# Kernel optimization log

Measured on AMD Instinct MI355X. Metric: run time of the kernel, lower is better.

Reference implementation:

```python
import jax, jax.numpy as jnp
import numpy as np

D = 512
H = 8
DK = D // H
EPS = 1e-5

def _layer_norm(x, w, b):
    mu = jnp.mean(x, axis=-1, keepdims=True)
    var = jnp.mean(jnp.square(x - mu), axis=-1, keepdims=True)
    return (x - mu) * jax.lax.rsqrt(var + EPS) * w + b

def setup_inputs() -> dict:
    key = jax.random.key(0)
    ks = jax.random.split(key, 16)
    B, S = 4, 2048
    s = 1.0 / np.sqrt(D)
    inp = {
        'q': jax.random.normal(ks[0], (B, S, D), jnp.float32),
        'k': jax.random.normal(ks[1], (B, S, D), jnp.float32),
        'v': jax.random.normal(ks[2], (B, S, D), jnp.float32),
        'mask': jnp.ones((S, S), jnp.int32),
        'pos_k': jax.random.normal(ks[3], (S, S), jnp.float32),
        'ln_w': jnp.ones((D,), jnp.float32),
        'ln_b': jnp.zeros((D,), jnp.float32),
        'Wq': jax.random.uniform(ks[4], (D, D), jnp.float32, -s, s),
        'bq': jax.random.uniform(ks[5], (D,), jnp.float32, -s, s),
        'Wk': jax.random.uniform(ks[6], (D, D), jnp.float32, -s, s),
        'bk': jax.random.uniform(ks[7], (D,), jnp.float32, -s, s),
        'Wv': jax.random.uniform(ks[8], (D, D), jnp.float32, -s, s),
        'bv': jax.random.uniform(ks[9], (D,), jnp.float32, -s, s),
        'Wo': jax.random.uniform(ks[10], (D, D), jnp.float32, -s, s),
        'bo': jax.random.uniform(ks[11], (D,), jnp.float32, -s, s),
    }
    return inp

def reference(q, k, v, mask, pos_k, ln_w, ln_b, Wq, bq, Wk, bk, Wv, bv, Wo, bo):
    B, S, _ = q.shape
    # shared LayerNorm on q, k, v
    qn = _layer_norm(q, ln_w, ln_b)
    kn = _layer_norm(k, ln_w, ln_b)
    vn = _layer_norm(v, ln_w, ln_b)
    # projections -> [B, H, S, DK]
    qh = (qn @ Wq.T + bq).reshape(B, S, H, DK).transpose(0, 2, 1, 3)
    kh = (kn @ Wk.T + bk).reshape(B, S, H, DK).transpose(0, 2, 1, 3)
    vh = (vn @ Wv.T + bv).reshape(B, S, H, DK).transpose(0, 2, 1, 3)
    scores = jnp.einsum('bhqd,bhkd->bhqk', qh, kh) / np.sqrt(DK)
    scores = scores + pos_k[None, None, :S, :S]
    scores = jnp.where(mask[None, None] == 0, -jnp.inf, scores)
    attn = jax.nn.softmax(scores, axis=-1)  # dropout is identity in eval
    x = jnp.einsum('bhqk,bhkd->bhqd', attn, vh).transpose(0, 2, 1, 3).reshape(B, S, D)
    out = x @ Wo.T + bo
    return out, attn
```

## Files before the change

### kernel.cpp

```cpp
#include <hip/hip_runtime.h>


typedef __bf16 bf16;
typedef __attribute__((ext_vector_type(8))) __bf16 bfv8;
typedef __attribute__((ext_vector_type(4))) __bf16 bfv4;
typedef __attribute__((ext_vector_type(4))) float  f32x4;

static constexpr int Dm = 512, Hh = 8, Sq = 2048, Bb = 4;
static constexpr int BS = Bb * Sq;

__device__ __forceinline__ f32x4 mfma16(bfv8 a, bfv8 b, f32x4 c) {
  return __builtin_amdgcn_mfma_f32_16x16x32_bf16(a, b, c, 0, 0, 0);
}

__global__ __launch_bounds__(256) void posT_kernel(
    const float* __restrict__ pos, const int* __restrict__ mask,
    float* __restrict__ posT) {
  __shared__ float tile[32][33];
  int i0 = blockIdx.y * 32, j0 = blockIdx.x * 32;
  int tx = threadIdx.x & 31, ty = threadIdx.x >> 5;
#pragma unroll
  for (int rr = 0; rr < 32; rr += 8) {
    int i = i0 + ty + rr, j = j0 + tx;
    float pv = pos[(size_t)i * Sq + j];
    int   mv = mask[(size_t)i * Sq + j];
    tile[ty + rr][tx] = mv ? pv : -1e30f;
  }
  __syncthreads();
#pragma unroll
  for (int rr = 0; rr < 32; rr += 8) {
    int j = j0 + ty + rr, i = i0 + tx;
    posT[(size_t)j * Sq + i] = tile[tx][ty + rr];
  }
}

__global__ __launch_bounds__(256) void ln_kernel(
    const float* __restrict__ q, const float* __restrict__ k,
    const float* __restrict__ v, const float* __restrict__ w,
    const float* __restrict__ bia, bf16* __restrict__ qn,
    bf16* __restrict__ kn, bf16* __restrict__ vn) {
  int wv = threadIdx.x >> 6, lane = threadIdx.x & 63;
  int row = blockIdx.x * 4 + wv;
  int which = blockIdx.y;
  const float* src = which == 0 ? q : (which == 1 ? k : v);
  bf16* dst        = which == 0 ? qn : (which == 1 ? kn : vn);

  f32x4 x0 = *(const f32x4*)(src + (size_t)row * Dm + lane * 8);
  f32x4 x1 = *(const f32x4*)(src + (size_t)row * Dm + lane * 8 + 4);
  float xf[8], s1 = 0.f, s2 = 0.f;
#pragma unroll
  for (int i = 0; i < 4; i++) { xf[i] = x0[i]; xf[4 + i] = x1[i]; }
#pragma unroll
  for (int i = 0; i < 8; i++) { s1 += xf[i]; s2 += xf[i] * xf[i]; }
#pragma unroll
  for (int m = 1; m < 64; m <<= 1) { s1 += __shfl_xor(s1, m, 64); s2 += __shfl_xor(s2, m, 64); }
  float mu = s1 * (1.0f / 512.0f);
  float var = s2 * (1.0f / 512.0f) - mu * mu;
  float rs = rsqrtf(var + 1e-5f);
  f32x4 w0 = *(const f32x4*)(w + lane * 8);
  f32x4 w1 = *(const f32x4*)(w + lane * 8 + 4);
  f32x4 b0 = *(const f32x4*)(bia + lane * 8);
  f32x4 b1 = *(const f32x4*)(bia + lane * 8 + 4);
  bfv8 o;
#pragma unroll
  for (int i = 0; i < 4; i++) {
    o[i]     = (bf16)((xf[i] - mu) * rs * w0[i] + b0[i]);
    o[4 + i] = (bf16)((xf[4 + i] - mu) * rs * w1[i] + b1[i]);
  }
  *(bfv8*)(dst + (size_t)row * Dm + lane * 8) = o;
}

__global__ __launch_bounds__(256) void gemm_bt(
    const bf16* __restrict__ A, const float* __restrict__ W,
    const float* __restrict__ bias, bf16* __restrict__ outb,
    float* __restrict__ outf, int mode) {
  __shared__ __align__(16) bf16 As[64][72];
  __shared__ __align__(16) bf16 Bs[64][72];
  int m0 = blockIdx.x * 64, n0 = blockIdx.y * 64;
  int tid = threadIdx.x;
  int wv = tid >> 6, lane = tid & 63;
  int wm = (wv & 1) * 32, wn = (wv >> 1) * 32;
  int r16 = lane & 15, quad = lane >> 4;
  int lr = tid >> 2, sc = (tid & 3) * 16;

  f32x4 acc[2][2] = {};
  const bf16*  Ap = A + (size_t)(m0 + lr) * 512 + sc;
  const float* Wp = W + (size_t)(n0 + lr) * 512 + sc;

  for (int k0 = 0; k0 < 512; k0 += 64) {
    bfv8 a0 = *(const bfv8*)(Ap + k0);
    bfv8 a1 = *(const bfv8*)(Ap + k0 + 8);
    f32x4 w0 = *(const f32x4*)(Wp + k0);
    f32x4 w1 = *(const f32x4*)(Wp + k0 + 4);
    f32x4 w2 = *(const f32x4*)(Wp + k0 + 8);
    f32x4 w3 = *(const f32x4*)(Wp + k0 + 12);
    bfv8 bb0, bb1;
#pragma unroll
    for (int i = 0; i < 4; i++) {
      bb0[i] = (bf16)w0[i]; bb0[4 + i] = (bf16)w1[i];
      bb1[i] = (bf16)w2[i]; bb1[4 + i] = (bf16)w3[i];
    }
    __syncthreads();
    *(bfv8*)&As[lr][sc] = a0;  *(bfv8*)&As[lr][sc + 8] = a1;
    *(bfv8*)&Bs[lr][sc] = bb0; *(bfv8*)&Bs[lr][sc + 8] = bb1;
    __syncthreads();
#pragma unroll
    for (int kk = 0; kk < 2; kk++) {
      bfv8 af0 = *(const bfv8*)&As[wm + r16][kk * 32 + quad * 8];
      bfv8 af1 = *(const bfv8*)&As[wm + 16 + r16][kk * 32 + quad * 8];
      bfv8 bf0 = *(const bfv8*)&Bs[wn + r16][kk * 32 + quad * 8];
      bfv8 bf1 = *(const bfv8*)&Bs[wn + 16 + r16][kk * 32 + quad * 8];
      acc[0][0] = mfma16(af0, bf0, acc[0][0]);
      acc[0][1] = mfma16(af0, bf1, acc[0][1]);
      acc[1][0] = mfma16(af1, bf0, acc[1][0]);
      acc[1][1] = mfma16(af1, bf1, acc[1][1]);
    }
  }

#pragma unroll
  for (int nt = 0; nt < 2; nt++) {
    int n = n0 + wn + nt * 16 + r16;
    float bb = bias[n];
#pragma unroll
    for (int mt = 0; mt < 2; mt++) {
#pragma unroll
      for (int r = 0; r < 4; r++) {
        int m = m0 + wm + mt * 16 + quad * 4 + r;
        float o = acc[mt][nt][r] + bb;
        int bb_ = m >> 11, s = m & 2047, hh = n >> 6, dd = n & 63;
        if (mode == 0)
          outb[(((size_t)(bb_ * Hh + hh)) * Sq + s) * 64 + dd] = (bf16)o;
        else if (mode == 1)
          outb[(((size_t)(bb_ * Hh + hh)) * 64 + dd) * Sq + s] = (bf16)o;
        else
          outf[(size_t)m * 512 + n] = o;
      }
    }
  }
}

__global__ __launch_bounds__(256, 2) void attn_kernel(
    const bf16* __restrict__ qh, const bf16* __restrict__ kh,
    const bf16* __restrict__ vT, const float* __restrict__ posT,
    float* __restrict__ attn, bf16* __restrict__ xout) {
  __shared__ float smax[4][16];
  __shared__ float ssum[4][16];
  __shared__ __align__(16) bf16 Pbuf[4][16][136];
  __shared__ __align__(16) float xred[4][16][64];

  const int tid = threadIdx.x;
  const int wv = tid >> 6, lane = tid & 63;
  const int r16 = lane & 15, quad = lane >> 4;
  const int strip = blockIdx.x, h = blockIdx.y, b = blockIdx.z;
  const int bh = b * Hh + h;
  const int r0 = strip * 16;
  const int c0 = wv * 512;

  const bf16* qbase = qh + (size_t)bh * Sq * 64;
  const bf16* kbase = kh + (size_t)bh * Sq * 64;
  const bf16* vbase = vT + (size_t)bh * 64 * Sq;

  bfv8 aq0 = *(const bfv8*)(qbase + (size_t)(r0 + r16) * 64 + quad * 8);
  bfv8 aq1 = *(const bfv8*)(qbase + (size_t)(r0 + r16) * 64 + 32 + quad * 8);

  f32x4 acc[32];
#pragma unroll
  for (int t = 0; t < 32; t++) {
    const bf16* kp = kbase + (size_t)(c0 + t * 16 + r16) * 64 + quad * 8;
    bfv8 b0 = *(const bfv8*)kp;
    bfv8 b1 = *(const bfv8*)(kp + 32);
    f32x4 z = {0.f, 0.f, 0.f, 0.f};
    z = mfma16(aq0, b0, z);
    z = mfma16(aq1, b1, z);
    acc[t] = z;
  }

  float mx[4] = {-1e30f, -1e30f, -1e30f, -1e30f};
#pragma unroll
  for (int t = 0; t < 32; t++) {
    int colg = c0 + t * 16 + r16;
    f32x4 pk = *(const f32x4*)(posT + (size_t)colg * Sq + r0 + quad * 4);
#pragma unroll
    for (int r = 0; r < 4; r++) {
      float s = acc[t][r] * 0.125f + pk[r];
      acc[t][r] = s;
      mx[r] = fmaxf(mx[r], s);
    }
  }
#pragma unroll
  for (int m = 1; m < 16; m <<= 1)
#pragma unroll
    for (int r = 0; r < 4; r++) mx[r] = fmaxf(mx[r], __shfl_xor(mx[r], m, 64));
  if (r16 == 0) {
#pragma unroll
    for (int r = 0; r < 4; r++) smax[wv][quad * 4 + r] = mx[r];
  }
  __syncthreads();
  float M[4];
#pragma unroll
  for (int r = 0; r < 4; r++) {
    int row = quad * 4 + r;
    M[r] = fmaxf(fmaxf(smax[0][row], smax[1][row]), fmaxf(smax[2][row], smax[3][row]));
  }

  float sm[4] = {0.f, 0.f, 0.f, 0.f};
#pragma unroll
  for (int t = 0; t < 32; t++)
#pragma unroll
    for (int r = 0; r < 4; r++) {
      float e = __expf(acc[t][r] - M[r]);
      acc[t][r] = e;
      sm[r] += e;
    }
#pragma unroll
  for (int m = 1; m < 16; m <<= 1)
#pragma unroll
    for (int r = 0; r < 4; r++) sm[r] += __shfl_xor(sm[r], m, 64);
  if (r16 == 0) {
#pragma unroll
    for (int r = 0; r < 4; r++) ssum[wv][quad * 4 + r] = sm[r];
  }
  __syncthreads();
  float inv[4];
#pragma unroll
  for (int r = 0; r < 4; r++) {
    int row = quad * 4 + r;
    inv[r] = 1.0f / (ssum[0][row] + ssum[1][row] + ssum[2][row] + ssum[3][row]);
  }

  f32x4 xacc[4] = {};
#pragma unroll
  for (int c = 0; c < 4; c++) {
#pragma unroll
    for (int tt = 0; tt < 8; tt++) {
      int t = c * 8 + tt;
      int colg = c0 + t * 16 + r16;
#pragma unroll
      for (int r = 0; r < 4; r++) {
        float p = acc[t][r] * inv[r];
        Pbuf[wv][quad * 4 + r][tt * 16 + r16] = (bf16)p;
        attn[((size_t)bh * Sq + r0 + quad * 4 + r) * Sq + colg] = p;
      }
    }
#pragma unroll
    for (int ks = 0; ks < 4; ks++) {
      bfv8 af = *(const bfv8*)&Pbuf[wv][r16][ks * 32 + quad * 8];
      int key0 = c0 + c * 128 + ks * 32;
#pragma unroll
      for (int nt = 0; nt < 4; nt++) {
        bfv8 bvv = *(const bfv8*)(vbase + (size_t)(nt * 16 + r16) * Sq + key0 + quad * 8);
        xacc[nt] = mfma16(af, bvv, xacc[nt]);
      }
    }
  }

#pragma unroll
  for (int nt = 0; nt < 4; nt++)
#pragma unroll
    for (int r = 0; r < 4; r++)
      xred[wv][quad * 4 + r][nt * 16 + r16] = xacc[nt][r];
  __syncthreads();
  {
    int row = tid >> 4, d4 = (tid & 15) * 4;
    f32x4 s0 = *(const f32x4*)&xred[0][row][d4];
    f32x4 s1 = *(const f32x4*)&xred[1][row][d4];
    f32x4 s2 = *(const f32x4*)&xred[2][row][d4];
    f32x4 s3 = *(const f32x4*)&xred[3][row][d4];
    f32x4 s = s0 + s1 + s2 + s3;
    bfv4 o;
#pragma unroll
    for (int i = 0; i < 4; i++) o[i] = (bf16)s[i];
    *(bfv4*)(xout + ((size_t)(b * Sq + r0 + row)) * 512 + h * 64 + d4) = o;
  }
}

extern "C" void kernel_launch(void* const* d_in, const int* in_sizes, int n_in,
                              void* d_out, int out_size, void* d_ws,
                              size_t ws_size, hipStream_t stream) {
  const float* q    = (const float*)d_in[0];
  const float* k    = (const float*)d_in[1];
  const float* v    = (const float*)d_in[2];
  const int*   mask = (const int*)d_in[3];
  const float* pos  = (const float*)d_in[4];
  const float* lnw  = (const float*)d_in[5];
  const float* lnb  = (const float*)d_in[6];
  const float* Wq   = (const float*)d_in[7];
  const float* bq   = (const float*)d_in[8];
  const float* Wk   = (const float*)d_in[9];
  const float* bk   = (const float*)d_in[10];
  const float* Wv   = (const float*)d_in[11];
  const float* bv   = (const float*)d_in[12];
  const float* Wo   = (const float*)d_in[13];
  const float* bo   = (const float*)d_in[14];

  const size_t NE = (size_t)Bb * Sq * Dm;
  if (ws_size < 64ull * 1024 * 1024) return;

  char* wsb = (char*)d_ws;
  float* posT = (float*)wsb;
  bf16* qn   = (bf16*)(wsb + 16ull * 1024 * 1024);
  bf16* kn   = (bf16*)(wsb + 24ull * 1024 * 1024);
  bf16* vn   = (bf16*)(wsb + 32ull * 1024 * 1024);
  bf16* qhp  = (bf16*)(wsb + 40ull * 1024 * 1024);
  bf16* khp  = (bf16*)(wsb + 48ull * 1024 * 1024);
  bf16* vhT  = (bf16*)(wsb + 56ull * 1024 * 1024);
  bf16* xbuf = qn;

  float* out  = (float*)d_out;
  float* attn = out + NE;

  posT_kernel<<<dim3(Sq / 32, Sq / 32), 256, 0, stream>>>(pos, mask, posT);
  ln_kernel<<<dim3(BS / 4, 3), 256, 0, stream>>>(q, k, v, lnw, lnb, qn, kn, vn);
  gemm_bt<<<dim3(BS / 64, Dm / 64), 256, 0, stream>>>(qn, Wq, bq, qhp, nullptr, 0);
  gemm_bt<<<dim3(BS / 64, Dm / 64), 256, 0, stream>>>(kn, Wk, bk, khp, nullptr, 0);
  gemm_bt<<<dim3(BS / 64, Dm / 64), 256, 0, stream>>>(vn, Wv, bv, vhT, nullptr, 1);
  attn_kernel<<<dim3(Sq / 16, Hh, Bb), 256, 0, stream>>>(qhp, khp, vhT, posT,
                                                         attn, xbuf);
  gemm_bt<<<dim3(BS / 64, Dm / 64), 256, 0, stream>>>(xbuf, Wo, bo, nullptr, out, 2);
}
```

Baseline: 1.036 ms.

## Split attention strip across eight waves with single-pass online softmax merge

After: 962.9 us. 7.0% less time.

```diff
diff --git a/kernel.cpp b/kernel.cpp
--- a/kernel.cpp
+++ b/kernel.cpp
@@ -4,7 +4,9 @@
 typedef __bf16 bf16;
 typedef __attribute__((ext_vector_type(8))) __bf16 bfv8;
 typedef __attribute__((ext_vector_type(4))) __bf16 bfv4;
+typedef __attribute__((ext_vector_type(2))) __bf16 bfv2;
 typedef __attribute__((ext_vector_type(4))) float  f32x4;
+typedef __attribute__((ext_vector_type(2))) float  f32x2;
 
 static constexpr int Dm = 512, Hh = 8, Sq = 2048, Bb = 4;
 static constexpr int BS = Bb * Sq;
@@ -139,14 +141,14 @@
   }
 }
 
-__global__ __launch_bounds__(256, 2) void attn_kernel(
+__global__ __launch_bounds__(512, 4) void attn_kernel(
     const bf16* __restrict__ qh, const bf16* __restrict__ kh,
     const bf16* __restrict__ vT, const float* __restrict__ posT,
     float* __restrict__ attn, bf16* __restrict__ xout) {
-  __shared__ float smax[4][16];
-  __shared__ float ssum[4][16];
-  __shared__ __align__(16) bf16 Pbuf[4][16][136];
-  __shared__ __align__(16) float xred[4][16][64];
+  __shared__ float smax[8][16];
+  __shared__ float ssum[8][16];
+  __shared__ __align__(16) bf16 Pbuf[8][16][136];
+  __shared__ __align__(16) float xred[8][16][64];
 
   const int tid = threadIdx.x;
   const int wv = tid >> 6, lane = tid & 63;
@@ -154,7 +156,7 @@
   const int strip = blockIdx.x, h = blockIdx.y, b = blockIdx.z;
   const int bh = b * Hh + h;
   const int r0 = strip * 16;
-  const int c0 = wv * 512;
+  const int c0 = wv * 256;
 
   const bf16* qbase = qh + (size_t)bh * Sq * 64;
   const bf16* kbase = kh + (size_t)bh * Sq * 64;
@@ -163,21 +165,21 @@
   bfv8 aq0 = *(const bfv8*)(qbase + (size_t)(r0 + r16) * 64 + quad * 8);
   bfv8 aq1 = *(const bfv8*)(qbase + (size_t)(r0 + r16) * 64 + 32 + quad * 8);
 
-  f32x4 acc[32];
-#pragma unroll
-  for (int t = 0; t < 32; t++) {
+  f32x4 acc[16];
+#pragma unroll
+  for (int t = 0; t < 16; t++) {
     const bf16* kp = kbase + (size_t)(c0 + t * 16 + r16) * 64 + quad * 8;
-    bfv8 b0 = *(const bfv8*)kp;
-    bfv8 b1 = *(const bfv8*)(kp + 32);
+    bfv8 kb0 = *(const bfv8*)kp;
+    bfv8 kb1 = *(const bfv8*)(kp + 32);
     f32x4 z = {0.f, 0.f, 0.f, 0.f};
-    z = mfma16(aq0, b0, z);
-    z = mfma16(aq1, b1, z);
+    z = mfma16(aq0, kb0, z);
+    z = mfma16(aq1, kb1, z);
     acc[t] = z;
   }
 
   float mx[4] = {-1e30f, -1e30f, -1e30f, -1e30f};
 #pragma unroll
-  for (int t = 0; t < 32; t++) {
+  for (int t = 0; t < 16; t++) {
     int colg = c0 + t * 16 + r16;
     f32x4 pk = *(const f32x4*)(posT + (size_t)colg * Sq + r0 + quad * 4);
 #pragma unroll
@@ -191,55 +193,56 @@
   for (int m = 1; m < 16; m <<= 1)
 #pragma unroll
     for (int r = 0; r < 4; r++) mx[r] = fmaxf(mx[r], __shfl_xor(mx[r], m, 64));
+
+  float sm[4] = {0.f, 0.f, 0.f, 0.f};
+#pragma unroll
+  for (int t = 0; t < 16; t++)
+#pragma unroll
+    for (int r = 0; r < 4; r++) {
+      float e = __expf(acc[t][r] - mx[r]);
+      acc[t][r] = e;
+      sm[r] += e;
+    }
+#pragma unroll
+  for (int m = 1; m < 16; m <<= 1)
+#pragma unroll
+    for (int r = 0; r < 4; r++) sm[r] += __shfl_xor(sm[r], m, 64);
+
   if (r16 == 0) {
 #pragma unroll
-    for (int r = 0; r < 4; r++) smax[wv][quad * 4 + r] = mx[r];
+    for (int r = 0; r < 4; r++) {
+      smax[wv][quad * 4 + r] = mx[r];
+      ssum[wv][quad * 4 + r] = sm[r];
+    }
   }
   __syncthreads();
-  float M[4];
+
+  float comb[4];
 #pragma unroll
   for (int r = 0; r < 4; r++) {
     int row = quad * 4 + r;
-    M[r] = fmaxf(fmaxf(smax[0][row], smax[1][row]), fmaxf(smax[2][row], smax[3][row]));
-  }
-
-  float sm[4] = {0.f, 0.f, 0.f, 0.f};
-#pragma unroll
-  for (int t = 0; t < 32; t++)
-#pragma unroll
-    for (int r = 0; r < 4; r++) {
-      float e = __expf(acc[t][r] - M[r]);
-      acc[t][r] = e;
-      sm[r] += e;
-    }
-#pragma unroll
-  for (int m = 1; m < 16; m <<= 1)
-#pragma unroll
-    for (int r = 0; r < 4; r++) sm[r] += __shfl_xor(sm[r], m, 64);
-  if (r16 == 0) {
-#pragma unroll
-    for (int r = 0; r < 4; r++) ssum[wv][quad * 4 + r] = sm[r];
-  }
-  __syncthreads();
-  float inv[4];
-#pragma unroll
-  for (int r = 0; r < 4; r++) {
-    int row = quad * 4 + r;
-    inv[r] = 1.0f / (ssum[0][row] + ssum[1][row] + ssum[2][row] + ssum[3][row]);
+    float M = smax[0][row];
+#pragma unroll
+    for (int w = 1; w < 8; w++) M = fmaxf(M, smax[w][row]);
+    float S = 0.f;
+#pragma unroll
+    for (int w = 0; w < 8; w++) S += ssum[w][row] * __expf(smax[w][row] - M);
+    comb[r] = __expf(mx[r] - M) / S;
   }
 
   f32x4 xacc[4] = {};
 #pragma unroll
-  for (int c = 0; c < 4; c++) {
+  for (int c = 0; c < 2; c++) {
 #pragma unroll
     for (int tt = 0; tt < 8; tt++) {
       int t = c * 8 + tt;
       int colg = c0 + t * 16 + r16;
 #pragma unroll
       for (int r = 0; r < 4; r++) {
-        float p = acc[t][r] * inv[r];
+        float p = acc[t][r] * comb[r];
         Pbuf[wv][quad * 4 + r][tt * 16 + r16] = (bf16)p;
-        attn[((size_t)bh * Sq + r0 + quad * 4 + r) * Sq + colg] = p;
+        __builtin_nontemporal_store(
+            p, attn + ((size_t)bh * Sq + r0 + quad * 4 + r) * Sq + colg);
       }
     }
 #pragma unroll
@@ -261,16 +264,14 @@
       xred[wv][quad * 4 + r][nt * 16 + r16] = xacc[nt][r];
   __syncthreads();
   {
-    int row = tid >> 4, d4 = (tid & 15) * 4;
-    f32x4 s0 = *(const f32x4*)&xred[0][row][d4];
-    f32x4 s1 = *(const f32x4*)&xred[1][row][d4];
-    f32x4 s2 = *(const f32x4*)&xred[2][row][d4];
-    f32x4 s3 = *(const f32x4*)&xred[3][row][d4];
-    f32x4 s = s0 + s1 + s2 + s3;
-    bfv4 o;
-#pragma unroll
-    for (int i = 0; i < 4; i++) o[i] = (bf16)s[i];
-    *(bfv4*)(xout + ((size_t)(b * Sq + r0 + row)) * 512 + h * 64 + d4) = o;
+    int row = tid >> 5, d2 = (tid & 31) * 2;
+    f32x2 s = {0.f, 0.f};
+#pragma unroll
+    for (int w = 0; w < 8; w++) s += *(const f32x2*)&xred[w][row][d2];
+    bfv2 o;
+    o[0] = (bf16)s[0];
+    o[1] = (bf16)s[1];
+    *(bfv2*)(xout + ((size_t)(b * Sq + r0 + row)) * 512 + h * 64 + d2) = o;
   }
 }
 
@@ -314,7 +315,7 @@
   gemm_bt<<<dim3(BS / 64, Dm / 64), 256, 0, stream>>>(qn, Wq, bq, qhp, nullptr, 0);
   gemm_bt<<<dim3(BS / 64, Dm / 64), 256, 0, stream>>>(kn, Wk, bk, khp, nullptr, 0);
   gemm_bt<<<dim3(BS / 64, Dm / 64), 256, 0, stream>>>(vn, Wv, bv, vhT, nullptr, 1);
-  attn_kernel<<<dim3(Sq / 16, Hh, Bb), 256, 0, stream>>>(qhp, khp, vhT, posT,
+  attn_kernel<<<dim3(Sq / 16, Hh, Bb), 512, 0, stream>>>(qhp, khp, vhT, posT,
                                                          attn, xbuf);
   gemm_bt<<<dim3(BS / 64, Dm / 64), 256, 0, stream>>>(xbuf, Wo, bo, nullptr, out, 2);
 }
```
